# Optimization experiments

Hardware: AMD Instinct MI355X
Metric: run time of the kernel (lower is better)

## Reference

```python
import jax, jax.numpy as jnp
import numpy as np

N_NODES = 50000
N_EDGES = 800000
NODE_IN, EDGE_IN, HIDDEN, OUT = 64, 16, 128, 32


def _gcn_conv(x, edge_index, W, b, num_nodes):
    """PyG GCNConv: symmetric-normalized aggregation with self-loops.
       out = D^{-1/2} (A + I) D^{-1/2} (x @ W) + b
    """
    h = x @ W                                   # [N, H]
    loop = jnp.arange(num_nodes, dtype=edge_index.dtype)
    row = jnp.concatenate([edge_index[0], loop])  # src
    col = jnp.concatenate([edge_index[1], loop])  # dst
    deg = jax.ops.segment_sum(jnp.ones(row.shape[0], dtype=h.dtype), col,
                              num_segments=num_nodes)
    dinv = jnp.where(deg > 0, jax.lax.rsqrt(deg), 0.0)
    norm = dinv[row] * dinv[col]                # [E+N]
    msg = h[row] * norm[:, None]                # gather + scale
    out = jax.ops.segment_sum(msg, col, num_segments=num_nodes)  # scatter-add
    return out + b


def setup_inputs() -> dict:
    key = jax.random.key(0)
    ks = jax.random.split(key, 8)
    s1 = 1.0 / np.sqrt(NODE_IN)
    s2 = 1.0 / np.sqrt(HIDDEN)
    s3 = 1.0 / np.sqrt(HIDDEN * 2 + EDGE_IN)
    return {
        "x": jax.random.normal(ks[0], (N_NODES, NODE_IN), dtype=jnp.float32),
        "edge_index": jax.random.randint(ks[1], (2, N_EDGES), 0, N_NODES,
                                         dtype=jnp.int64),
        "edge_attr": jax.random.normal(ks[2], (N_EDGES, EDGE_IN),
                                       dtype=jnp.float32),
        "W1": jax.random.normal(ks[3], (NODE_IN, HIDDEN), dtype=jnp.float32) * s1,
        "b1": jnp.zeros((HIDDEN,), dtype=jnp.float32),
        "W2": jax.random.normal(ks[4], (HIDDEN, HIDDEN), dtype=jnp.float32) * s2,
        "b2": jnp.zeros((HIDDEN,), dtype=jnp.float32),
        "W_edge": jax.random.normal(ks[5], (HIDDEN * 2 + EDGE_IN, OUT),
                                    dtype=jnp.float32) * s3,
        "b_edge": jnp.zeros((OUT,), dtype=jnp.float32),
    }


def reference(x, edge_index, edge_attr, W1, b1, W2, b2, W_edge, b_edge):
    n = x.shape[0]
    h = jax.nn.relu(_gcn_conv(x, edge_index, W1, b1, n))
    h = jax.nn.relu(_gcn_conv(h, edge_index, W2, b2, n))
    src, dst = edge_index[0], edge_index[1]
    edge_features = jnp.concatenate([h[src], h[dst], edge_attr], axis=1)
    return edge_features @ W_edge + b_edge
```

## Files before the change

kernel.cpp:

```cpp
#include <hip/hip_runtime.h>

#define NN 50000
#define NE 800000

typedef __attribute__((ext_vector_type(8))) short short8v;
typedef __attribute__((ext_vector_type(4))) float f32x4;

__device__ __forceinline__ float bf_lo(unsigned u) { return __uint_as_float(u << 16); }
__device__ __forceinline__ float bf_hi(unsigned u) { return __uint_as_float(u & 0xffff0000u); }
__device__ __forceinline__ unsigned pack_bf2(float a, float b) {
  unsigned ua = __float_as_uint(a);
  ua = (ua + 0x7fffu + ((ua >> 16) & 1u)) >> 16;
  unsigned ub = __float_as_uint(b);
  ub = (ub + 0x7fffu + ((ub >> 16) & 1u)) & 0xffff0000u;
  return ua | ub;
}
__device__ __forceinline__ unsigned short bf16r(float f) {
  unsigned u = __float_as_uint(f);
  u = (u + 0x7fffu + ((u >> 16) & 1u)) >> 16;
  return (unsigned short)u;
}

__global__ void k_zero(int* cnt, int* cur, int n) {
  int i = blockIdx.x * blockDim.x + threadIdx.x;
  if (i < n) { cnt[i] = 0; cur[i] = 0; }
}

__global__ void k_count(const int* dst, int* cnt, int e) {
  int i = blockIdx.x * blockDim.x + threadIdx.x;
  if (i < e) atomicAdd(&cnt[dst[i]], 1);
}

__global__ void k_scan1(const int* cnt, int* offs, int* bsum, int n) {
  __shared__ int s[256];
  int i = blockIdx.x * 256 + threadIdx.x;
  int v = (i < n) ? cnt[i] : 0;
  s[threadIdx.x] = v;
  __syncthreads();
  #pragma unroll
  for (int d = 1; d < 256; d <<= 1) {
    int t = (threadIdx.x >= d) ? s[threadIdx.x - d] : 0;
    __syncthreads();
    s[threadIdx.x] += t;
    __syncthreads();
  }
  if (i < n) offs[i] = s[threadIdx.x] - v;
  if (threadIdx.x == 255) bsum[blockIdx.x] = s[255];
}

__global__ void k_scan2(int* bsum, int* offsN, int nb) {
  __shared__ int s[256];
  int v = (threadIdx.x < nb) ? bsum[threadIdx.x] : 0;
  s[threadIdx.x] = v;
  __syncthreads();
  #pragma unroll
  for (int d = 1; d < 256; d <<= 1) {
    int t = (threadIdx.x >= d) ? s[threadIdx.x - d] : 0;
    __syncthreads();
    s[threadIdx.x] += t;
    __syncthreads();
  }
  if (threadIdx.x < nb) bsum[threadIdx.x] = s[threadIdx.x] - v;
  if (threadIdx.x == 255) *offsN = s[255];
}

__global__ void k_scan3_dinv(int* offs, const int* bsum, const int* cnt,
                             float* dinv, int n) {
  int i = blockIdx.x * blockDim.x + threadIdx.x;
  if (i < n) {
    offs[i] += bsum[i >> 8];
    dinv[i] = rsqrtf((float)(cnt[i] + 1));
  }
}

__global__ void k_fill(const int* src, const int* dst, const int* offs,
                       int* cur, int* adj, int e) {
  int i = blockIdx.x * blockDim.x + threadIdx.x;
  if (i < e) {
    int d = dst[i];
    int pos = atomicAdd(&cur[d], 1);
    adj[offs[d] + pos] = src[i];
  }
}

__global__ void k_prepw(const float* __restrict__ W1, const float* __restrict__ W2,
                        unsigned short* __restrict__ W1t,
                        unsigned short* __restrict__ W2t) {
  int i = blockIdx.x * 256 + threadIdx.x;
  if (i < 8192)  { int c = i >> 6, k = i & 63;  W1t[i] = bf16r(W1[k * 128 + c]); }
  if (i < 16384) { int c = i >> 7, k = i & 127; W2t[i] = bf16r(W2[k * 128 + c]); }
}

__global__ void k_prescale(const float* __restrict__ x,
                           const float* __restrict__ dinv,
                           unsigned* __restrict__ xs, int n) {
  int i = blockIdx.x * blockDim.x + threadIdx.x;
  if (i >= n * 32) return;
  int v = i >> 5, c2 = i & 31;
  float d = dinv[v];
  float2 xv = ((const float2*)(x + (size_t)v * 64))[c2];
  xs[(size_t)v * 32 + c2] = pack_bf2(xv.x * d, xv.y * d);
}

__global__ void k_agg64(const unsigned* __restrict__ xs,
                        const int* __restrict__ offs, const int* __restrict__ adj,
                        const float* __restrict__ dinv, unsigned* __restrict__ z,
                        int n) {
  int node = blockIdx.x * 8 + (threadIdx.x >> 5);
  if (node >= n) return;
  int lane = threadIdx.x & 31;
  float ax[8], ay[8];
  {
    unsigned u = xs[(size_t)node * 32 + lane];
    ax[0] = bf_lo(u); ay[0] = bf_hi(u);
  }
  #pragma unroll
  for (int u = 1; u < 8; u++) { ax[u] = 0.f; ay[u] = 0.f; }
  int s = offs[node], e = offs[node + 1];
  int i = s;
  for (; i + 8 <= e; i += 8) {
    int idx[8];
    #pragma unroll
    for (int u = 0; u < 8; u++) idx[u] = adj[i + u];
    #pragma unroll
    for (int u = 0; u < 8; u++) {
      unsigned uv = xs[(size_t)idx[u] * 32 + lane];
      ax[u] += bf_lo(uv); ay[u] += bf_hi(uv);
    }
  }
  for (; i < e; i++) {
    unsigned uv = xs[(size_t)adj[i] * 32 + lane];
    ax[0] += bf_lo(uv); ay[0] += bf_hi(uv);
  }
  float sx = ((ax[0] + ax[1]) + (ax[2] + ax[3])) + ((ax[4] + ax[5]) + (ax[6] + ax[7]));
  float sy = ((ay[0] + ay[1]) + (ay[2] + ay[3])) + ((ay[4] + ay[5]) + (ay[6] + ay[7]));
  float d = dinv[node];
  z[(size_t)node * 32 + lane] = pack_bf2(sx * d, sy * d);
}

__global__ void k_agg128(const unsigned* __restrict__ hs,
                         const int* __restrict__ offs, const int* __restrict__ adj,
                         const float* __restrict__ dinv, unsigned* __restrict__ z,
                         int n) {
  int node = blockIdx.x * 4 + (threadIdx.x >> 6);
  if (node >= n) return;
  int lane = threadIdx.x & 63;
  float ax[8], ay[8];
  {
    unsigned u = hs[(size_t)node * 64 + lane];
    ax[0] = bf_lo(u); ay[0] = bf_hi(u);
  }
  #pragma unroll
  for (int u = 1; u < 8; u++) { ax[u] = 0.f; ay[u] = 0.f; }
  int s = offs[node], e = offs[node + 1];
  int i = s;
  for (; i + 8 <= e; i += 8) {
    int idx[8];
    #pragma unroll
    for (int u = 0; u < 8; u++) idx[u] = adj[i + u];
    #pragma unroll
    for (int u = 0; u < 8; u++) {
      unsigned uv = hs[(size_t)idx[u] * 64 + lane];
      ax[u] += bf_lo(uv); ay[u] += bf_hi(uv);
    }
  }
  for (; i < e; i++) {
    unsigned uv = hs[(size_t)adj[i] * 64 + lane];
    ax[0] += bf_lo(uv); ay[0] += bf_hi(uv);
  }
  float sx = ((ax[0] + ax[1]) + (ax[2] + ax[3])) + ((ax[4] + ax[5]) + (ax[6] + ax[7]));
  float sy = ((ay[0] + ay[1]) + (ay[2] + ay[3])) + ((ay[4] + ay[5]) + (ay[6] + ay[7]));
  float d = dinv[node];
  z[(size_t)node * 64 + lane] = pack_bf2(sx * d, sy * d);
}

template <int K, int EPI>
__global__ __launch_bounds__(256) void k_mgemm(const unsigned short* __restrict__ A,
                                               const unsigned short* __restrict__ Bt,
                                               const float* __restrict__ bias,
                                               const float* __restrict__ dinv,
                                               float* __restrict__ outf,
                                               unsigned short* __restrict__ outb,
                                               int n) {
  int lane = threadIdx.x & 63;
  int wid = threadIdx.x >> 6;
  int wr = wid >> 1;
  int wc = wid & 1;
  int r0 = blockIdx.x * 32 + wr * 16;
  int cbase = wc * 64;
  int lr = lane & 15;
  int lk = (lane >> 4) * 8;
  int arow = r0 + lr;
  if (arow >= n) arow = n - 1;
  const unsigned short* arp = A + (size_t)arow * K + lk;
  f32x4 acc[4];
  #pragma unroll
  for (int ct = 0; ct < 4; ct++) acc[ct] = (f32x4){0.f, 0.f, 0.f, 0.f};
  #pragma unroll
  for (int ks = 0; ks < K; ks += 32) {
    short8v a = *reinterpret_cast<const short8v*>(arp + ks);
    #pragma unroll
    for (int ct = 0; ct < 4; ct++) {
      const unsigned short* bp = Bt + (size_t)(cbase + ct * 16 + lr) * K + lk + ks;
      short8v b = *reinterpret_cast<const short8v*>(bp);
      acc[ct] = __builtin_amdgcn_mfma_f32_16x16x32_bf16(a, b, acc[ct], 0, 0, 0);
    }
  }
  int rbase = r0 + (lane >> 4) * 4;
  #pragma unroll
  for (int ct = 0; ct < 4; ct++) {
    int col = cbase + ct * 16 + lr;
    float bv = bias[col];
    #pragma unroll
    for (int rg = 0; rg < 4; rg++) {
      int row = rbase + rg;
      if (row >= n) continue;
      float v = fmaxf(acc[ct][rg] + bv, 0.f);
      if (EPI == 0) {
        outb[(size_t)row * 128 + col] = bf16r(v * dinv[row]);
      } else {
        outf[(size_t)row * 128 + col] = v;
      }
    }
  }
}

__global__ __launch_bounds__(256) void k_pq2(const float* __restrict__ H,
                                             const float* __restrict__ We,
                                             float* __restrict__ PQ, int n) {
  const int ROWS = 32;
  __shared__ float hsm[ROWS][128];
  __shared__ float wl[128][64];
  int r0 = blockIdx.x * ROWS;
  int col = threadIdx.x & 63;
  int rg = threadIdx.x >> 6;
  for (int idx = threadIdx.x; idx < 1024; idx += 256) {
    int r = idx >> 5, k4 = idx & 31;
    int gr = r0 + r;
    float4 v = make_float4(0.f, 0.f, 0.f, 0.f);
    if (gr < n) v = ((const float4*)(H + (size_t)gr * 128))[k4];
    ((float4*)hsm[r])[k4] = v;
  }
  for (int idx = threadIdx.x; idx < 2048; idx += 256) {
    int k = idx >> 4, c4 = idx & 15;
    int c = c4 * 4;
    float4 v;
    if (c < 32)
      v = *(const float4*)(We + (size_t)k * 32 + c);
    else
      v = *(const float4*)(We + (size_t)(128 + k) * 32 + (c - 32));
    ((float4*)wl[k])[c4] = v;
  }
  __syncthreads();
  float acc[8];
  #pragma unroll
  for (int i = 0; i < 8; i++) acc[i] = 0.f;
  #pragma unroll 4
  for (int kk = 0; kk < 128; kk += 4) {
    float w0 = wl[kk + 0][col];
    float w1 = wl[kk + 1][col];
    float w2 = wl[kk + 2][col];
    float w3 = wl[kk + 3][col];
    #pragma unroll
    for (int r = 0; r < 8; r++) {
      float4 xv = *(const float4*)&hsm[rg * 8 + r][kk];
      acc[r] += xv.x * w0 + xv.y * w1 + xv.z * w2 + xv.w * w3;
    }
  }
  #pragma unroll
  for (int r = 0; r < 8; r++) {
    int gr = r0 + rg * 8 + r;
    if (gr < n) PQ[(size_t)gr * 64 + col] = acc[r];
  }
}

__global__ __launch_bounds__(256) void k_edge4(const int* __restrict__ src,
                                               const int* __restrict__ dst,
                                               const float* __restrict__ ea,
                                               const float* __restrict__ PQ,
                                               const float* __restrict__ We,
                                               const float* __restrict__ be,
                                               float* __restrict__ out, int ne) {
  __shared__ int sidx[64];
  __shared__ int didx[64];
  __shared__ float eas[64][16];
  __shared__ float wcs[16][32];
  __shared__ float bes[32];
  int tid = threadIdx.x;
  int ebase = blockIdx.x * 64;
  if (tid < 128)
    ((float4*)wcs)[tid] = ((const float4*)(We + 256 * 32))[tid];
  if (tid < 32) bes[tid] = be[tid];
  if (tid >= 128 && tid < 192) sidx[tid - 128] = src[ebase + tid - 128];
  if (tid >= 192)              didx[tid - 192] = dst[ebase + tid - 192];
  {
    int row = tid >> 2, q = tid & 3;
    ((float4*)eas[row])[q] = ((const float4*)(ea + (size_t)(ebase + row) * 16))[q];
  }
  __syncthreads();
  int j = tid & 31;
  int grp = tid >> 5;
  float pv[8], qv[8];
  int el[8];
  #pragma unroll
  for (int u = 0; u < 8; u++) el[u] = u * 8 + grp;
  #pragma unroll
  for (int u = 0; u < 8; u++) {
    int s = sidx[el[u]];
    int d = didx[el[u]];
    pv[u] = PQ[(size_t)s * 64 + j];
    qv[u] = PQ[(size_t)d * 64 + 32 + j];
  }
  #pragma unroll
  for (int u = 0; u < 8; u++) {
    int e = ebase + el[u];
    float acc = pv[u] + qv[u] + bes[j];
    #pragma unroll
    for (int k = 0; k < 16; k++)
      acc += eas[el[u]][k] * wcs[k][j];
    out[(size_t)e * 32 + j] = acc;
  }
}

extern "C" void kernel_launch(void* const* d_in, const int* in_sizes, int n_in,
                              void* d_out, int out_size, void* d_ws, size_t ws_size,
                              hipStream_t stream) {
  const float* x  = (const float*)d_in[0];
  const int*   ei = (const int*)d_in[1];
  const float* ea = (const float*)d_in[2];
  const float* W1 = (const float*)d_in[3];
  const float* b1 = (const float*)d_in[4];
  const float* W2 = (const float*)d_in[5];
  const float* b2 = (const float*)d_in[6];
  const float* We = (const float*)d_in[7];
  const float* be = (const float*)d_in[8];
  float* out = (float*)d_out;
  const int* src = ei;
  const int* dst = ei + NE;

  char* w = (char*)d_ws;
  auto alloc = [&](size_t b) {
    void* p = (void*)w;
    w += (b + 255) & ~(size_t)255;
    return p;
  };
  int* cnt    = (int*)alloc(NN * 4);
  int* cur    = (int*)alloc(NN * 4);
  int* offs   = (int*)alloc((NN + 1) * 4);
  int* bsum   = (int*)alloc(256 * 4);
  int* adj    = (int*)alloc((size_t)NE * 4);
  float* dinv = (float*)alloc(NN * 4);
  unsigned* xs  = (unsigned*)alloc((size_t)NN * 32 * 4);
  unsigned* h1s = (unsigned*)alloc((size_t)NN * 64 * 4);
  unsigned* z12 = (unsigned*)alloc((size_t)NN * 64 * 4);
  float* h2   = (float*)alloc((size_t)NN * 128 * 4);
  unsigned short* w1t = (unsigned short*)alloc(8192 * 2);
  unsigned short* w2t = (unsigned short*)alloc(16384 * 2);
  float* pq   = (float*)h1s;

  const int nblkN = (NN + 255) / 256;
  const int nblkE = (NE + 255) / 256;

  k_zero<<<nblkN, 256, 0, stream>>>(cnt, cur, NN);
  k_count<<<nblkE, 256, 0, stream>>>(dst, cnt, NE);
  k_scan1<<<nblkN, 256, 0, stream>>>(cnt, offs, bsum, NN);
  k_scan2<<<1, 256, 0, stream>>>(bsum, offs + NN, nblkN);
  k_scan3_dinv<<<nblkN, 256, 0, stream>>>(offs, bsum, cnt, dinv, NN);
  k_fill<<<nblkE, 256, 0, stream>>>(src, dst, offs, cur, adj, NE);

  k_prepw<<<64, 256, 0, stream>>>(W1, W2, w1t, w2t);
  k_prescale<<<(NN * 32 + 255) / 256, 256, 0, stream>>>(x, dinv, xs, NN);
  k_agg64<<<(NN + 7) / 8, 256, 0, stream>>>(xs, offs, adj, dinv, z12, NN);

  const int mgBlk = (NN + 31) / 32;
  k_mgemm<64, 0><<<mgBlk, 256, 0, stream>>>((const unsigned short*)z12, w1t, b1,
                                            dinv, nullptr, (unsigned short*)h1s, NN);
  k_agg128<<<(NN + 3) / 4, 256, 0, stream>>>(h1s, offs, adj, dinv, z12, NN);
  k_mgemm<128, 1><<<mgBlk, 256, 0, stream>>>((const unsigned short*)z12, w2t, b2,
                                             nullptr, h2, nullptr, NN);

  k_pq2<<<mgBlk, 256, 0, stream>>>(h2, We, pq, NN);
  k_edge4<<<NE / 64, 256, 0, stream>>>(src, dst, ea, pq, We, be, out, NE);
}
```

Before: 281.3 us.

## Fuse layer-2 GEMM with edge projection via MFMA and store PQ in bf16

The second GCN GEMM now keeps its ReLU output in shared memory as bf16 and immediately runs a second MFMA GEMM against the transposed source/destination edge weights. This removes the fp32 h2 round trip through global memory and the separate scalar-FMA k_pq2 kernel. PQ is stored in bf16, which halves the random-gather traffic in the edge kernel, and the edge kernel now processes two output columns per thread. Zeroing and weight-prep kernels are merged into one launch. The cost is extra bf16 rounding of h2 and PQ, which lowers precision.

```diff
diff --git a/kernel.cpp b/kernel.cpp
--- a/kernel.cpp
+++ b/kernel.cpp
@@ -21,9 +21,21 @@
   return (unsigned short)u;
 }
 
-__global__ void k_zero(int* cnt, int* cur, int n) {
-  int i = blockIdx.x * blockDim.x + threadIdx.x;
-  if (i < n) { cnt[i] = 0; cur[i] = 0; }
+__global__ void k_prep0(const float* __restrict__ W1, const float* __restrict__ W2,
+                        const float* __restrict__ We,
+                        unsigned short* __restrict__ W1t,
+                        unsigned short* __restrict__ W2t,
+                        unsigned short* __restrict__ Wabt,
+                        int* cnt, int* cur) {
+  int i = blockIdx.x * 256 + threadIdx.x;
+  if (i < NN) { cnt[i] = 0; cur[i] = 0; }
+  if (i < 8192)  { int c = i >> 6, k = i & 63;  W1t[i] = bf16r(W1[k * 128 + c]); }
+  if (i < 16384) { int c = i >> 7, k = i & 127; W2t[i] = bf16r(W2[k * 128 + c]); }
+  if (i < 8192) {
+    int c = i >> 7, k = i & 127;
+    float v = (c < 32) ? We[k * 32 + c] : We[(128 + k) * 32 + (c - 32)];
+    Wabt[i] = bf16r(v);
+  }
 }
 
 __global__ void k_count(const int* dst, int* cnt, int e) {
@@ -81,14 +93,6 @@
     int pos = atomicAdd(&cur[d], 1);
     adj[offs[d] + pos] = src[i];
   }
-}
-
-__global__ void k_prepw(const float* __restrict__ W1, const float* __restrict__ W2,
-                        unsigned short* __restrict__ W1t,
-                        unsigned short* __restrict__ W2t) {
-  int i = blockIdx.x * 256 + threadIdx.x;
-  if (i < 8192)  { int c = i >> 6, k = i & 63;  W1t[i] = bf16r(W1[k * 128 + c]); }
-  if (i < 16384) { int c = i >> 7, k = i & 127; W2t[i] = bf16r(W2[k * 128 + c]); }
 }
 
 __global__ void k_prescale(const float* __restrict__ x,
@@ -174,18 +178,16 @@
   z[(size_t)node * 64 + lane] = pack_bf2(sx * d, sy * d);
 }
 
-template <int K, int EPI>
+template <int K>
 __global__ __launch_bounds__(256) void k_mgemm(const unsigned short* __restrict__ A,
                                                const unsigned short* __restrict__ Bt,
                                                const float* __restrict__ bias,
                                                const float* __restrict__ dinv,
-                                               float* __restrict__ outf,
                                                unsigned short* __restrict__ outb,
                                                int n) {
   int lane = threadIdx.x & 63;
   int wid = threadIdx.x >> 6;
-  int wr = wid >> 1;
-  int wc = wid & 1;
+  int wr = wid >> 1, wc = wid & 1;
   int r0 = blockIdx.x * 32 + wr * 16;
   int cbase = wc * 64;
   int lr = lane & 15;
@@ -216,68 +218,79 @@
       int row = rbase + rg;
       if (row >= n) continue;
       float v = fmaxf(acc[ct][rg] + bv, 0.f);
-      if (EPI == 0) {
-        outb[(size_t)row * 128 + col] = bf16r(v * dinv[row]);
-      } else {
-        outf[(size_t)row * 128 + col] = v;
-      }
-    }
-  }
-}
-
-__global__ __launch_bounds__(256) void k_pq2(const float* __restrict__ H,
-                                             const float* __restrict__ We,
-                                             float* __restrict__ PQ, int n) {
-  const int ROWS = 32;
-  __shared__ float hsm[ROWS][128];
-  __shared__ float wl[128][64];
-  int r0 = blockIdx.x * ROWS;
-  int col = threadIdx.x & 63;
-  int rg = threadIdx.x >> 6;
-  for (int idx = threadIdx.x; idx < 1024; idx += 256) {
-    int r = idx >> 5, k4 = idx & 31;
-    int gr = r0 + r;
-    float4 v = make_float4(0.f, 0.f, 0.f, 0.f);
-    if (gr < n) v = ((const float4*)(H + (size_t)gr * 128))[k4];
-    ((float4*)hsm[r])[k4] = v;
-  }
-  for (int idx = threadIdx.x; idx < 2048; idx += 256) {
-    int k = idx >> 4, c4 = idx & 15;
-    int c = c4 * 4;
-    float4 v;
-    if (c < 32)
-      v = *(const float4*)(We + (size_t)k * 32 + c);
-    else
-      v = *(const float4*)(We + (size_t)(128 + k) * 32 + (c - 32));
-    ((float4*)wl[k])[c4] = v;
+      outb[(size_t)row * 128 + col] = bf16r(v * dinv[row]);
+    }
+  }
+}
+
+__global__ __launch_bounds__(256) void k_mgemm2pq(
+    const unsigned short* __restrict__ A,
+    const unsigned short* __restrict__ Bt,
+    const unsigned short* __restrict__ Wabt,
+    const float* __restrict__ bias,
+    unsigned short* __restrict__ PQb,
+    int n) {
+  __shared__ unsigned short hs[32][136];
+  int lane = threadIdx.x & 63;
+  int wid = threadIdx.x >> 6;
+  int wr = wid >> 1, wc = wid & 1;
+  int r0 = blockIdx.x * 32;
+  int lr = lane & 15;
+  int lk = (lane >> 4) * 8;
+  int arow = r0 + wr * 16 + lr;
+  if (arow >= n) arow = n - 1;
+  const unsigned short* arp = A + (size_t)arow * 128 + lk;
+  f32x4 acc[4];
+  #pragma unroll
+  for (int ct = 0; ct < 4; ct++) acc[ct] = (f32x4){0.f, 0.f, 0.f, 0.f};
+  #pragma unroll
+  for (int ks = 0; ks < 128; ks += 32) {
+    short8v a = *reinterpret_cast<const short8v*>(arp + ks);
+    #pragma unroll
+    for (int ct = 0; ct < 4; ct++) {
+      const unsigned short* bp = Bt + (size_t)(wc * 64 + ct * 16 + lr) * 128 + lk + ks;
+      short8v b = *reinterpret_cast<const short8v*>(bp);
+      acc[ct] = __builtin_amdgcn_mfma_f32_16x16x32_bf16(a, b, acc[ct], 0, 0, 0);
+    }
+  }
+  int rloc = wr * 16 + (lane >> 4) * 4;
+  #pragma unroll
+  for (int ct = 0; ct < 4; ct++) {
+    int col = wc * 64 + ct * 16 + lr;
+    float bv = bias[col];
+    #pragma unroll
+    for (int rg = 0; rg < 4; rg++)
+      hs[rloc + rg][col] = bf16r(fmaxf(acc[ct][rg] + bv, 0.f));
   }
   __syncthreads();
-  float acc[8];
-  #pragma unroll
-  for (int i = 0; i < 8; i++) acc[i] = 0.f;
-  #pragma unroll 4
-  for (int kk = 0; kk < 128; kk += 4) {
-    float w0 = wl[kk + 0][col];
-    float w1 = wl[kk + 1][col];
-    float w2 = wl[kk + 2][col];
-    float w3 = wl[kk + 3][col];
-    #pragma unroll
-    for (int r = 0; r < 8; r++) {
-      float4 xv = *(const float4*)&hsm[rg * 8 + r][kk];
-      acc[r] += xv.x * w0 + xv.y * w1 + xv.z * w2 + xv.w * w3;
-    }
-  }
-  #pragma unroll
-  for (int r = 0; r < 8; r++) {
-    int gr = r0 + rg * 8 + r;
-    if (gr < n) PQ[(size_t)gr * 64 + col] = acc[r];
-  }
-}
-
-__global__ __launch_bounds__(256) void k_edge4(const int* __restrict__ src,
+  f32x4 acc2[2];
+  acc2[0] = (f32x4){0.f, 0.f, 0.f, 0.f};
+  acc2[1] = (f32x4){0.f, 0.f, 0.f, 0.f};
+  #pragma unroll
+  for (int ks = 0; ks < 128; ks += 32) {
+    short8v a2 = *reinterpret_cast<const short8v*>(&hs[wr * 16 + lr][lk + ks]);
+    #pragma unroll
+    for (int ct = 0; ct < 2; ct++) {
+      const unsigned short* wp = Wabt + (size_t)(wc * 32 + ct * 16 + lr) * 128 + lk + ks;
+      short8v b = *reinterpret_cast<const short8v*>(wp);
+      acc2[ct] = __builtin_amdgcn_mfma_f32_16x16x32_bf16(a2, b, acc2[ct], 0, 0, 0);
+    }
+  }
+  #pragma unroll
+  for (int ct = 0; ct < 2; ct++) {
+    int col = wc * 32 + ct * 16 + lr;
+    #pragma unroll
+    for (int rg = 0; rg < 4; rg++) {
+      int row = r0 + wr * 16 + (lane >> 4) * 4 + rg;
+      if (row < n) PQb[(size_t)row * 64 + col] = bf16r(acc2[ct][rg]);
+    }
+  }
+}
+
+__global__ __launch_bounds__(256) void k_edge5(const int* __restrict__ src,
                                                const int* __restrict__ dst,
                                                const float* __restrict__ ea,
-                                               const float* __restrict__ PQ,
+                                               const unsigned* __restrict__ PQw,
                                                const float* __restrict__ We,
                                                const float* __restrict__ be,
                                                float* __restrict__ out, int ne) {
@@ -298,27 +311,32 @@
     ((float4*)eas[row])[q] = ((const float4*)(ea + (size_t)(ebase + row) * 16))[q];
   }
   __syncthreads();
-  int j = tid & 31;
-  int grp = tid >> 5;
-  float pv[8], qv[8];
-  int el[8];
-  #pragma unroll
-  for (int u = 0; u < 8; u++) el[u] = u * 8 + grp;
-  #pragma unroll
-  for (int u = 0; u < 8; u++) {
+  int l = tid & 15;
+  int grp = tid >> 4;
+  unsigned pw[4], qw[4];
+  int el[4];
+  #pragma unroll
+  for (int u = 0; u < 4; u++) el[u] = u * 16 + grp;
+  #pragma unroll
+  for (int u = 0; u < 4; u++) {
     int s = sidx[el[u]];
     int d = didx[el[u]];
-    pv[u] = PQ[(size_t)s * 64 + j];
-    qv[u] = PQ[(size_t)d * 64 + 32 + j];
-  }
-  #pragma unroll
-  for (int u = 0; u < 8; u++) {
+    pw[u] = PQw[(size_t)s * 32 + l];
+    qw[u] = PQw[(size_t)d * 32 + 16 + l];
+  }
+  int c0 = 2 * l;
+  #pragma unroll
+  for (int u = 0; u < 4; u++) {
     int e = ebase + el[u];
-    float acc = pv[u] + qv[u] + bes[j];
-    #pragma unroll
-    for (int k = 0; k < 16; k++)
-      acc += eas[el[u]][k] * wcs[k][j];
-    out[(size_t)e * 32 + j] = acc;
+    float a0 = bf_lo(pw[u]) + bf_lo(qw[u]) + bes[c0];
+    float a1 = bf_hi(pw[u]) + bf_hi(qw[u]) + bes[c0 + 1];
+    #pragma unroll
+    for (int k = 0; k < 16; k++) {
+      float ev = eas[el[u]][k];
+      a0 += ev * wcs[k][c0];
+      a1 += ev * wcs[k][c0 + 1];
+    }
+    ((float2*)(out + (size_t)e * 32))[l] = make_float2(a0, a1);
   }
 }
 
@@ -353,32 +371,30 @@
   unsigned* xs  = (unsigned*)alloc((size_t)NN * 32 * 4);
   unsigned* h1s = (unsigned*)alloc((size_t)NN * 64 * 4);
   unsigned* z12 = (unsigned*)alloc((size_t)NN * 64 * 4);
-  float* h2   = (float*)alloc((size_t)NN * 128 * 4);
-  unsigned short* w1t = (unsigned short*)alloc(8192 * 2);
-  unsigned short* w2t = (unsigned short*)alloc(16384 * 2);
-  float* pq   = (float*)h1s;
+  unsigned short* w1t  = (unsigned short*)alloc(8192 * 2);
+  unsigned short* w2t  = (unsigned short*)alloc(16384 * 2);
+  unsigned short* wabt = (unsigned short*)alloc(8192 * 2);
+  unsigned short* pqb = (unsigned short*)h1s;
 
   const int nblkN = (NN + 255) / 256;
   const int nblkE = (NE + 255) / 256;
 
-  k_zero<<<nblkN, 256, 0, stream>>>(cnt, cur, NN);
+  k_prep0<<<nblkN, 256, 0, stream>>>(W1, W2, We, w1t, w2t, wabt, cnt, cur);
   k_count<<<nblkE, 256, 0, stream>>>(dst, cnt, NE);
   k_scan1<<<nblkN, 256, 0, stream>>>(cnt, offs, bsum, NN);
   k_scan2<<<1, 256, 0, stream>>>(bsum, offs + NN, nblkN);
   k_scan3_dinv<<<nblkN, 256, 0, stream>>>(offs, bsum, cnt, dinv, NN);
   k_fill<<<nblkE, 256, 0, stream>>>(src, dst, offs, cur, adj, NE);
 
-  k_prepw<<<64, 256, 0, stream>>>(W1, W2, w1t, w2t);
   k_prescale<<<(NN * 32 + 255) / 256, 256, 0, stream>>>(x, dinv, xs, NN);
   k_agg64<<<(NN + 7) / 8, 256, 0, stream>>>(xs, offs, adj, dinv, z12, NN);
 
   const int mgBlk = (NN + 31) / 32;
-  k_mgemm<64, 0><<<mgBlk, 256, 0, stream>>>((const unsigned short*)z12, w1t, b1,
-                                            dinv, nullptr, (unsigned short*)h1s, NN);
+  k_mgemm<64><<<mgBlk, 256, 0, stream>>>((const unsigned short*)z12, w1t, b1,
+                                         dinv, (unsigned short*)h1s, NN);
   k_agg128<<<(NN + 3) / 4, 256, 0, stream>>>(h1s, offs, adj, dinv, z12, NN);
-  k_mgemm<128, 1><<<mgBlk, 256, 0, stream>>>((const unsigned short*)z12, w2t, b2,
-                                             nullptr, h2, nullptr, NN);
-
-  k_pq2<<<mgBlk, 256, 0, stream>>>(h2, We, pq, NN);
-  k_edge4<<<NE / 64, 256, 0, stream>>>(src, dst, ea, pq, We, be, out, NE);
-}
+  k_mgemm2pq<<<mgBlk, 256, 0, stream>>>((const unsigned short*)z12, w2t, wabt,
+                                        b2, pqb, NN);
+  k_edge5<<<NE / 64, 256, 0, stream>>>(src, dst, ea, (const unsigned*)pqb,
+                                       We, be, out, NE);
+}
```

Measured after the change: 243.9 us. 1.15x faster.
